# Optimization experiments

Measured on AMD Instinct MI355X. Metric: run time of the kernel, lower is better.

Reference implementation:

```python
import jax, jax.numpy as jnp
import numpy as np

B, T, D, H = 8, 4096, 1024, 64


def setup_inputs() -> dict:
    key = jax.random.key(0)
    ks = jax.random.split(key, 16)
    s = 0.02
    return {
        "x": jax.random.normal(ks[0], (B, T, D), jnp.float32),
        "norm_w": jnp.ones((D,), jnp.float32),
        "W1": jax.random.normal(ks[1], (D, D), jnp.float32) * s,
        "W2": jax.random.normal(ks[2], (D, D), jnp.float32) * s,
        "Wlast": jax.random.normal(ks[3], (D, D), jnp.float32) * s,
        "conv_w": jax.random.normal(ks[4], (D, 3), jnp.float32) * s,  # depthwise k=3, tap 0 = oldest
        "conv_b": jnp.zeros((D,), jnp.float32),
        "A": jnp.log(jnp.arange(1, H + 1, dtype=jnp.float32)),
        "Bw": jax.random.normal(ks[5], (H, D), jnp.float32) * s,
        "Bb": jnp.zeros((H,), jnp.float32),
        "Cw": jax.random.normal(ks[6], (D, H), jnp.float32) * s,
        "Cb": jnp.zeros((D,), jnp.float32),
        "Dw": jax.random.normal(ks[7], (D, D), jnp.float32) * s,
        "Db": jnp.zeros((D,), jnp.float32),
        "dw": jax.random.normal(ks[8], (H, D), jnp.float32) * s,
        "db": jnp.zeros((H,), jnp.float32),
    }


def reference(x, norm_w, W1, W2, Wlast, conv_w, conv_b, A, Bw, Bb, Cw, Cb, Dw, Db, dw, db):
    eps = jnp.finfo(x.dtype).eps  # torch RMSNorm default eps
    res = x
    xn = x * jax.lax.rsqrt(jnp.mean(x * x, axis=-1, keepdims=True) + eps) * norm_w
    x_b = xn @ W1.T
    z = xn @ W2.T
    # causal depthwise conv, kernel_size=3, left-pad 2
    xp = jnp.pad(x_b, ((0, 0), (2, 0), (0, 0)))
    xc = xp[:, :-2] * conv_w[:, 0] + xp[:, 1:-1] * conv_w[:, 1] + xp[:, 2:] * conv_w[:, 2] + conv_b
    xc = jax.nn.silu(xc)
    # log-space selective scan (cumprod(exp(A)) == exp(cumsum(A)))
    delta = jax.nn.softplus(xc @ dw.T + db)          # (B,T,H)
    A_log = -jax.nn.softplus(A)                      # (H,)
    A_bar_log = delta * A_log
    B_bar = delta * (xc @ Bw.T + Bb)
    A_cum = jnp.clip(jnp.cumsum(A_bar_log, axis=1), -20.0, 20.0)
    A_shift = jnp.concatenate([jnp.zeros_like(A_cum[:, :1]), A_cum[:, :-1]], axis=1)
    h = jnp.exp(A_cum) * jnp.cumsum(B_bar * jnp.exp(-A_shift), axis=1)
    y = h @ Cw.T + Cb + (xc @ Dw.T + Db)
    out = (y * jax.nn.silu(z)) @ Wlast.T + res
    return out
```

## Files before the change

kernel.cpp:

```cpp
#include <hip/hip_runtime.h>
#include <stdint.h>
#include <stddef.h>

#define TDIM 4096
#define DDIM 1024
#define HDIM 64
#define BDIM 8
#define MROWS (BDIM * TDIM)
#define KCAT (DDIM + HDIM)

typedef unsigned short ushort_t;
typedef __attribute__((ext_vector_type(8))) short short8;
typedef __attribute__((ext_vector_type(4))) float floatx4;

__device__ __forceinline__ unsigned short f2bf(float f) {
  unsigned u = __float_as_uint(f);
  u += 0x7fffu + ((u >> 16) & 1u);
  return (unsigned short)(u >> 16);
}
__device__ __forceinline__ float bf2f(unsigned short s) {
  return __uint_as_float(((unsigned)s) << 16);
}
__device__ __forceinline__ float softplusf(float x) {
  return x > 20.f ? x : log1pf(expf(x));
}

__global__ void k_cvt(const float* __restrict__ src, ushort_t* __restrict__ dst, int n) {
  int i = blockIdx.x * blockDim.x + threadIdx.x;
  if (i < n) dst[i] = f2bf(src[i]);
}

__global__ void k_bcat(const float* __restrict__ Dw, const float* __restrict__ Cw,
                       ushort_t* __restrict__ bcat) {
  int i = blockIdx.x * blockDim.x + threadIdx.x;
  if (i >= DDIM * KCAT) return;
  int row = i / KCAT, k = i - row * KCAT;
  float v = (k < DDIM) ? Dw[row * DDIM + k] : Cw[row * HDIM + (k - DDIM)];
  bcat[i] = f2bf(v);
}

__global__ void k_bias(const float* __restrict__ Cb, const float* __restrict__ Db,
                       float* __restrict__ biasCD) {
  int i = blockIdx.x * blockDim.x + threadIdx.x;
  if (i < DDIM) biasCD[i] = Cb[i] + Db[i];
}

__global__ __launch_bounds__(256) void k_rms(const float* __restrict__ x,
                                             const float* __restrict__ nw,
                                             ushort_t* __restrict__ xn) {
  const int row = blockIdx.x;
  const int tid = threadIdx.x;
  const size_t base = (size_t)row * DDIM + tid * 4;
  const float4 xv = *(const float4*)(x + base);
  float ss = xv.x * xv.x + xv.y * xv.y + xv.z * xv.z + xv.w * xv.w;
  for (int off = 32; off > 0; off >>= 1) ss += __shfl_down(ss, off, 64);
  __shared__ float sws[4];
  const int lane = tid & 63, w = tid >> 6;
  if (lane == 0) sws[w] = ss;
  __syncthreads();
  const float tot = sws[0] + sws[1] + sws[2] + sws[3];
  const float scale = rsqrtf(tot * (1.0f / DDIM) + 1.1920929e-7f);
  const float4 nwv = *(const float4*)(nw + tid * 4);
  ushort4 o;
  o.x = f2bf(xv.x * scale * nwv.x);
  o.y = f2bf(xv.y * scale * nwv.y);
  o.z = f2bf(xv.z * scale * nwv.z);
  o.w = f2bf(xv.w * scale * nwv.w);
  *(ushort4*)(xn + base) = o;
}

__global__ __launch_bounds__(256) void k_conv(const ushort_t* __restrict__ xz,
                                              const float* __restrict__ cw,
                                              const float* __restrict__ cb,
                                              ushort_t* __restrict__ acat) {
  const size_t idx = (size_t)blockIdx.x * 256 + threadIdx.x;
  const int d = (int)(idx & (DDIM - 1));
  const size_t m = idx >> 10;
  const int t = (int)(m & (TDIM - 1));
  const size_t s = m * 2048 + d;
  const float w0 = cw[d * 3 + 0], w1 = cw[d * 3 + 1], w2 = cw[d * 3 + 2];
  float v = bf2f(xz[s]) * w2;
  if (t >= 1) v += bf2f(xz[s - 2048]) * w1;
  if (t >= 2) v += bf2f(xz[s - 4096]) * w0;
  v += cb[d];
  const float sv = v / (1.f + __expf(-v));
  acat[m * KCAT + d] = f2bf(sv);
}

__global__ __launch_bounds__(256) void k_scan(const float* __restrict__ preG,
                                              const float* __restrict__ db,
                                              const float* __restrict__ Bb,
                                              const float* __restrict__ A,
                                              ushort_t* __restrict__ hT) {
  const int ch = blockIdx.x;
  const int b = ch >> 6, h = ch & 63;
  const int tid = threadIdx.x;
  const float dbh = db[h], Bbh = Bb[h];
  const float al = -softplusf(A[h]);
  const size_t base = ((size_t)b * TDIM + (size_t)tid * 16) * 128 + h;

  float a[16], bbv[16];
#pragma unroll
  for (int k = 0; k < 16; ++k) {
    const float p1 = preG[base + (size_t)k * 128];
    const float p2 = preG[base + (size_t)k * 128 + 64];
    const float delta = softplusf(p1 + dbh);
    a[k] = delta * al;
    bbv[k] = delta * (p2 + Bbh);
  }
  float run = 0.f;
#pragma unroll
  for (int k = 0; k < 16; ++k) { run += a[k]; a[k] = run; }

  __shared__ float sh[256];
  sh[tid] = run;
  __syncthreads();
  for (int s = 1; s < 256; s <<= 1) {
    float v = (tid >= s) ? sh[tid - s] : 0.f;
    __syncthreads();
    sh[tid] += v;
    __syncthreads();
  }
  const float off = (tid > 0) ? sh[tid - 1] : 0.f;
  __syncthreads();

  float term[16];
  float prev = off;
#pragma unroll
  for (int k = 0; k < 16; ++k) {
    const float Pk = off + a[k];
    const float Ashift = fminf(fmaxf(prev, -20.f), 20.f);
    term[k] = bbv[k] * expf(-Ashift);
    a[k] = fminf(fmaxf(Pk, -20.f), 20.f);
    prev = Pk;
  }

  float run2 = 0.f;
#pragma unroll
  for (int k = 0; k < 16; ++k) { run2 += term[k]; term[k] = run2; }
  sh[tid] = run2;
  __syncthreads();
  for (int s = 1; s < 256; s <<= 1) {
    float v = (tid >= s) ? sh[tid - s] : 0.f;
    __syncthreads();
    sh[tid] += v;
    __syncthreads();
  }
  const float off2 = (tid > 0) ? sh[tid - 1] : 0.f;

  ushort_t* dst = hT + (size_t)h * MROWS + (size_t)b * TDIM + (size_t)tid * 16;
#pragma unroll
  for (int k = 0; k < 16; ++k) {
    dst[k] = f2bf(expf(a[k]) * (off2 + term[k]));
  }
}

__global__ __launch_bounds__(256) void k_htrans(const ushort_t* __restrict__ hT,
                                                ushort_t* __restrict__ acat) {
  __shared__ ushort_t t[64 * 256];
  const int tid = threadIdx.x;
  const int m0 = blockIdx.x * 256;
#pragma unroll
  for (int p = 0; p < 8; ++p) {
    const int e = p * 2048 + tid * 8;
    const int h = e >> 8, mm = e & 255;
    *(short8*)(t + e) = *(const short8*)(hT + (size_t)h * MROWS + m0 + mm);
  }
  __syncthreads();
  ushort_t* dst = acat + (size_t)(m0 + tid) * KCAT + DDIM;
#pragma unroll
  for (int p = 0; p < 8; ++p) {
    short8 v;
#pragma unroll
    for (int e = 0; e < 8; ++e) v[e] = t[(p * 8 + e) * 256 + tid];
    *(short8*)(dst + p * 8) = v;
  }
}

__device__ __forceinline__ void stage128x64(const ushort_t* __restrict__ G, int row0,
                                            int ld, int kc, ushort_t* s, int wave, int lane) {
  const int rsub = lane >> 3;
  const int cpos = lane & 7;
  using gp_t = const unsigned int __attribute__((address_space(1)))*;
  using lp_t = unsigned int __attribute__((address_space(3)))*;
#pragma unroll
  for (int g = 0; g < 4; ++g) {
    const int rg = wave * 4 + g;
    const int r = rg * 8 + rsub;
    const int c = cpos ^ rsub;
    const ushort_t* src = G + (size_t)(row0 + r) * (size_t)ld + (size_t)(kc + c * 8);
    __builtin_amdgcn_global_load_lds((gp_t)(const void*)src, (lp_t)(void*)(s + rg * 512),
                                     16, 0, 0);
  }
}

__global__ __launch_bounds__(256, 3) void k_gemm(
    const ushort_t* __restrict__ A, int lda,
    const ushort_t* __restrict__ Bt, int ldb,
    int nB, int Kdim, int mode,
    float* __restrict__ outF, ushort_t* __restrict__ outB, int ldc,
    const float* __restrict__ bias,
    const ushort_t* __restrict__ zmat, int ldz,
    const float* __restrict__ resid) {
  __shared__ alignas(16) ushort_t smem[128 * 128];
  ushort_t* sA = smem;
  ushort_t* sB = smem + 128 * 64;
  const int tid = threadIdx.x;
  const int wave = tid >> 6, lane = tid & 63;

  const int per = gridDim.x >> 3;
  const int xcd = blockIdx.x & 7, slot = blockIdx.x >> 3;
  const int tile = xcd * per + slot;
  const int m0 = (tile / nB) * 128, n0 = (tile % nB) * 128;

  const int half_m = (wave & 1) * 64, half_n = (wave >> 1) * 64;
  const int quad = lane >> 4, l16 = lane & 15;

  floatx4 acc[4][4];
#pragma unroll
  for (int i = 0; i < 4; ++i)
#pragma unroll
    for (int j = 0; j < 4; ++j) acc[i][j] = floatx4{0.f, 0.f, 0.f, 0.f};

  for (int kc = 0; kc < Kdim; kc += 64) {
    stage128x64(A, m0, lda, kc, sA, wave, lane);
    stage128x64(Bt, n0, ldb, kc, sB, wave, lane);
    __syncthreads();
#pragma unroll
    for (int s = 0; s < 2; ++s) {
      short8 af[4], bfr[4];
#pragma unroll
      for (int i = 0; i < 4; ++i) {
        const int r = half_m + i * 16 + l16;
        const int cp = (s * 4 + quad) ^ (r & 7);
        af[i] = *(const short8*)(sA + r * 64 + cp * 8);
      }
#pragma unroll
      for (int j = 0; j < 4; ++j) {
        const int r = half_n + j * 16 + l16;
        const int cp = (s * 4 + quad) ^ (r & 7);
        bfr[j] = *(const short8*)(sB + r * 64 + cp * 8);
      }
#pragma unroll
      for (int i = 0; i < 4; ++i)
#pragma unroll
        for (int j = 0; j < 4; ++j)
          acc[i][j] = __builtin_amdgcn_mfma_f32_16x16x32_bf16(af[i], bfr[j], acc[i][j], 0, 0, 0);
    }
    __syncthreads();
  }

#pragma unroll
  for (int i = 0; i < 4; ++i)
#pragma unroll
    for (int j = 0; j < 4; ++j)
#pragma unroll
      for (int rg = 0; rg < 4; ++rg) {
        const int r = half_m + i * 16 + quad * 4 + rg;
        const int c = half_n + j * 16 + l16;
        smem[r * 128 + c] = f2bf(acc[i][j][rg]);
      }
  __syncthreads();

#pragma unroll
  for (int p = 0; p < 8; ++p) {
    const int r = p * 16 + (tid >> 4);
    const int c = (tid & 15) * 8;
    short8 v8 = *(const short8*)(smem + r * 128 + c);
    const size_t m = (size_t)(m0 + r);
    const int n = n0 + c;
    if (mode == 0) {
      *(short8*)(outB + m * (size_t)ldc + n) = v8;
    } else if (mode == 1) {
      float* o = outF + m * (size_t)ldc + n;
#pragma unroll
      for (int e = 0; e < 8; ++e) o[e] = bf2f((ushort_t)v8[e]);
    } else if (mode == 2) {
      const short8 z8 = *(const short8*)(zmat + m * (size_t)ldz + n);
      short8 o;
#pragma unroll
      for (int e = 0; e < 8; ++e) {
        const float v = bf2f((ushort_t)v8[e]) + bias[n + e];
        const float zf = bf2f((ushort_t)z8[e]);
        o[e] = (short)f2bf(v * (zf / (1.f + __expf(-zf))));
      }
      *(short8*)(outB + m * (size_t)ldc + n) = o;
    } else {
      const float* rs = resid + m * (size_t)ldc + n;
      float* o = outF + m * (size_t)ldc + n;
#pragma unroll
      for (int e = 0; e < 8; ++e) o[e] = bf2f((ushort_t)v8[e]) + rs[e];
    }
  }
}

extern "C" void kernel_launch(void* const* d_in, const int* in_sizes, int n_in,
                              void* d_out, int out_size, void* d_ws, size_t ws_size,
                              hipStream_t stream) {
  const float* x      = (const float*)d_in[0];
  const float* norm_w = (const float*)d_in[1];
  const float* W1     = (const float*)d_in[2];
  const float* W2     = (const float*)d_in[3];
  const float* Wlast  = (const float*)d_in[4];
  const float* conv_w = (const float*)d_in[5];
  const float* conv_b = (const float*)d_in[6];
  const float* Aarr   = (const float*)d_in[7];
  const float* Bw     = (const float*)d_in[8];
  const float* Bb     = (const float*)d_in[9];
  const float* Cw     = (const float*)d_in[10];
  const float* Cb     = (const float*)d_in[11];
  const float* Dw     = (const float*)d_in[12];
  const float* Db     = (const float*)d_in[13];
  const float* dwm    = (const float*)d_in[14];
  const float* dbv    = (const float*)d_in[15];

  char* ws = (char*)d_ws;
  ushort_t* xz   = (ushort_t*)(ws + 0);
  ushort_t* acat = (ushort_t*)(ws + 134217728);
  float*   preG  = (float*)(ws + 205520896);
  ushort_t* hT   = (ushort_t*)(ws + 222298112);
  ushort_t* xnu  = (ushort_t*)(ws + 226492416);
  ushort_t* wcat = (ushort_t*)(ws + 293601280);
  ushort_t* wlb  = (ushort_t*)(ws + 297795584);
  ushort_t* dwbw = (ushort_t*)(ws + 299892736);
  ushort_t* bcat = (ushort_t*)(ws + 300154880);
  float*  biasCD = (float*)(ws + 302383104);
  float*   outF  = (float*)d_out;

  k_cvt<<<4096, 256, 0, stream>>>(W1, wcat, DDIM * DDIM);
  k_cvt<<<4096, 256, 0, stream>>>(W2, wcat + DDIM * DDIM, DDIM * DDIM);
  k_cvt<<<4096, 256, 0, stream>>>(Wlast, wlb, DDIM * DDIM);
  k_cvt<<<256, 256, 0, stream>>>(dwm, dwbw, HDIM * DDIM);
  k_cvt<<<256, 256, 0, stream>>>(Bw, dwbw + HDIM * DDIM, HDIM * DDIM);
  k_bcat<<<(DDIM * KCAT + 255) / 256, 256, 0, stream>>>(Dw, Cw, bcat);
  k_bias<<<4, 256, 0, stream>>>(Cb, Db, biasCD);

  k_rms<<<MROWS, 256, 0, stream>>>(x, norm_w, xnu);

  k_gemm<<<256 * 16, 256, 0, stream>>>(xnu, DDIM, wcat, DDIM, 16, DDIM, 0,
                                       nullptr, xz, 2048, nullptr, nullptr, 0, nullptr);

  k_conv<<<(MROWS * DDIM) / 256, 256, 0, stream>>>(xz, conv_w, conv_b, acat);

  k_gemm<<<256 * 1, 256, 0, stream>>>(acat, KCAT, dwbw, DDIM, 1, DDIM, 1,
                                      preG, nullptr, 128, nullptr, nullptr, 0, nullptr);

  k_scan<<<BDIM * HDIM, 256, 0, stream>>>(preG, dbv, Bb, Aarr, hT);

  k_htrans<<<MROWS / 256, 256, 0, stream>>>(hT, acat);

  k_gemm<<<256 * 8, 256, 0, stream>>>(acat, KCAT, bcat, KCAT, 8, KCAT, 2,
                                      nullptr, xnu, DDIM, biasCD, xz + DDIM, 2048, nullptr);

  k_gemm<<<256 * 8, 256, 0, stream>>>(xnu, DDIM, wlb, DDIM, 8, DDIM, 3,
                                      outF, nullptr, DDIM, nullptr, nullptr, 0, x);

  (void)in_sizes; (void)n_in; (void)out_size; (void)ws_size;
}
```

Baseline: 761.8 us.

## Fuse weight prep, vectorize conv, transpose delta/B GEMM output, raise occupancy

Merges the seven weight-conversion and bias launches into one prep kernel. Vectorizes the depthwise conv to process eight channels per thread with 16-byte loads and stores. Swaps the operands of the small delta/B projection GEMM so its output is laid out channel-major (H x M), which lets the scan read contiguous float4s instead of strided scalars. It also raises the GEMM launch-bounds occupancy hint from 3 to 4 blocks per SIMD, which may increase register pressure or spills in the large GEMMs.

```diff
diff --git a/kernel.cpp b/kernel.cpp
--- a/kernel.cpp
+++ b/kernel.cpp
@@ -8,6 +8,8 @@
 #define BDIM 8
 #define MROWS (BDIM * TDIM)
 #define KCAT (DDIM + HDIM)
+#define DD (DDIM * DDIM)
+#define HD (HDIM * DDIM)
 
 typedef unsigned short ushort_t;
 typedef __attribute__((ext_vector_type(8))) short short8;
@@ -25,23 +27,32 @@
   return x > 20.f ? x : log1pf(expf(x));
 }
 
-__global__ void k_cvt(const float* __restrict__ src, ushort_t* __restrict__ dst, int n) {
-  int i = blockIdx.x * blockDim.x + threadIdx.x;
-  if (i < n) dst[i] = f2bf(src[i]);
-}
-
-__global__ void k_bcat(const float* __restrict__ Dw, const float* __restrict__ Cw,
-                       ushort_t* __restrict__ bcat) {
-  int i = blockIdx.x * blockDim.x + threadIdx.x;
-  if (i >= DDIM * KCAT) return;
-  int row = i / KCAT, k = i - row * KCAT;
-  float v = (k < DDIM) ? Dw[row * DDIM + k] : Cw[row * HDIM + (k - DDIM)];
-  bcat[i] = f2bf(v);
-}
-
-__global__ void k_bias(const float* __restrict__ Cb, const float* __restrict__ Db,
+__global__ void k_prep(const float* __restrict__ W1, const float* __restrict__ W2,
+                       const float* __restrict__ Wlast, const float* __restrict__ dwm,
+                       const float* __restrict__ Bw, const float* __restrict__ Dw,
+                       const float* __restrict__ Cw, const float* __restrict__ Cb,
+                       const float* __restrict__ Db,
+                       ushort_t* __restrict__ wcat, ushort_t* __restrict__ wlb,
+                       ushort_t* __restrict__ dwbw, ushort_t* __restrict__ bcat,
                        float* __restrict__ biasCD) {
-  int i = blockIdx.x * blockDim.x + threadIdx.x;
+  int i = blockIdx.x * 256 + threadIdx.x;
+  if (i < DD) { wcat[i] = f2bf(W1[i]); return; }
+  i -= DD;
+  if (i < DD) { wcat[DD + i] = f2bf(W2[i]); return; }
+  i -= DD;
+  if (i < DD) { wlb[i] = f2bf(Wlast[i]); return; }
+  i -= DD;
+  if (i < HD) { dwbw[i] = f2bf(dwm[i]); return; }
+  i -= HD;
+  if (i < HD) { dwbw[HD + i] = f2bf(Bw[i]); return; }
+  i -= HD;
+  if (i < DDIM * KCAT) {
+    const int row = i / KCAT, k = i - row * KCAT;
+    const float v = (k < DDIM) ? Dw[row * DDIM + k] : Cw[row * HDIM + (k - DDIM)];
+    bcat[i] = f2bf(v);
+    return;
+  }
+  i -= DDIM * KCAT;
   if (i < DDIM) biasCD[i] = Cb[i] + Db[i];
 }
 
@@ -73,18 +84,26 @@
                                               const float* __restrict__ cw,
                                               const float* __restrict__ cb,
                                               ushort_t* __restrict__ acat) {
-  const size_t idx = (size_t)blockIdx.x * 256 + threadIdx.x;
-  const int d = (int)(idx & (DDIM - 1));
-  const size_t m = idx >> 10;
+  const size_t eidx = ((size_t)blockIdx.x * 256 + threadIdx.x) * 8;
+  const int d = (int)(eidx & (DDIM - 1));
+  const size_t m = eidx >> 10;
   const int t = (int)(m & (TDIM - 1));
   const size_t s = m * 2048 + d;
-  const float w0 = cw[d * 3 + 0], w1 = cw[d * 3 + 1], w2 = cw[d * 3 + 2];
-  float v = bf2f(xz[s]) * w2;
-  if (t >= 1) v += bf2f(xz[s - 2048]) * w1;
-  if (t >= 2) v += bf2f(xz[s - 4096]) * w0;
-  v += cb[d];
-  const float sv = v / (1.f + __expf(-v));
-  acat[m * KCAT + d] = f2bf(sv);
+  const short8 r2 = *(const short8*)(xz + s);
+  short8 r1 = {0,0,0,0,0,0,0,0}, r0 = {0,0,0,0,0,0,0,0};
+  if (t >= 1) r1 = *(const short8*)(xz + s - 2048);
+  if (t >= 2) r0 = *(const short8*)(xz + s - 4096);
+  short8 o;
+#pragma unroll
+  for (int e = 0; e < 8; ++e) {
+    const int de = d + e;
+    float v = bf2f((ushort_t)r2[e]) * cw[de * 3 + 2]
+            + bf2f((ushort_t)r1[e]) * cw[de * 3 + 1]
+            + bf2f((ushort_t)r0[e]) * cw[de * 3 + 0]
+            + cb[de];
+    o[e] = (short)f2bf(v / (1.f + __expf(-v)));
+  }
+  *(short8*)(acat + m * KCAT + d) = o;
 }
 
 __global__ __launch_bounds__(256) void k_scan(const float* __restrict__ preG,
@@ -97,16 +116,22 @@
   const int tid = threadIdx.x;
   const float dbh = db[h], Bbh = Bb[h];
   const float al = -softplusf(A[h]);
-  const size_t base = ((size_t)b * TDIM + (size_t)tid * 16) * 128 + h;
+  const size_t base1 = (size_t)h * MROWS + (size_t)b * TDIM + (size_t)tid * 16;
+  const size_t base2 = base1 + (size_t)64 * MROWS;
 
   float a[16], bbv[16];
 #pragma unroll
-  for (int k = 0; k < 16; ++k) {
-    const float p1 = preG[base + (size_t)k * 128];
-    const float p2 = preG[base + (size_t)k * 128 + 64];
-    const float delta = softplusf(p1 + dbh);
-    a[k] = delta * al;
-    bbv[k] = delta * (p2 + Bbh);
+  for (int k4 = 0; k4 < 4; ++k4) {
+    const float4 p1 = *(const float4*)(preG + base1 + k4 * 4);
+    const float4 p2 = *(const float4*)(preG + base2 + k4 * 4);
+    const float pp1[4] = {p1.x, p1.y, p1.z, p1.w};
+    const float pp2[4] = {p2.x, p2.y, p2.z, p2.w};
+#pragma unroll
+    for (int e = 0; e < 4; ++e) {
+      const float delta = softplusf(pp1[e] + dbh);
+      a[k4 * 4 + e] = delta * al;
+      bbv[k4 * 4 + e] = delta * (pp2[e] + Bbh);
+    }
   }
   float run = 0.f;
 #pragma unroll
@@ -194,7 +219,7 @@
   }
 }
 
-__global__ __launch_bounds__(256, 3) void k_gemm(
+__global__ __launch_bounds__(256, 4) void k_gemm(
     const ushort_t* __restrict__ A, int lda,
     const ushort_t* __restrict__ Bt, int ldb,
     int nB, int Kdim, int mode,
@@ -327,23 +352,21 @@
   float*  biasCD = (float*)(ws + 302383104);
   float*   outF  = (float*)d_out;
 
-  k_cvt<<<4096, 256, 0, stream>>>(W1, wcat, DDIM * DDIM);
-  k_cvt<<<4096, 256, 0, stream>>>(W2, wcat + DDIM * DDIM, DDIM * DDIM);
-  k_cvt<<<4096, 256, 0, stream>>>(Wlast, wlb, DDIM * DDIM);
-  k_cvt<<<256, 256, 0, stream>>>(dwm, dwbw, HDIM * DDIM);
-  k_cvt<<<256, 256, 0, stream>>>(Bw, dwbw + HDIM * DDIM, HDIM * DDIM);
-  k_bcat<<<(DDIM * KCAT + 255) / 256, 256, 0, stream>>>(Dw, Cw, bcat);
-  k_bias<<<4, 256, 0, stream>>>(Cb, Db, biasCD);
+  {
+    const int total = 3 * DD + 2 * HD + DDIM * KCAT + DDIM;
+    k_prep<<<(total + 255) / 256, 256, 0, stream>>>(W1, W2, Wlast, dwm, Bw, Dw, Cw, Cb, Db,
+                                                    wcat, wlb, dwbw, bcat, biasCD);
+  }
 
   k_rms<<<MROWS, 256, 0, stream>>>(x, norm_w, xnu);
 
   k_gemm<<<256 * 16, 256, 0, stream>>>(xnu, DDIM, wcat, DDIM, 16, DDIM, 0,
                                        nullptr, xz, 2048, nullptr, nullptr, 0, nullptr);
 
-  k_conv<<<(MROWS * DDIM) / 256, 256, 0, stream>>>(xz, conv_w, conv_b, acat);
-
-  k_gemm<<<256 * 1, 256, 0, stream>>>(acat, KCAT, dwbw, DDIM, 1, DDIM, 1,
-                                      preG, nullptr, 128, nullptr, nullptr, 0, nullptr);
+  k_conv<<<(MROWS * DDIM) / (256 * 8), 256, 0, stream>>>(xz, conv_w, conv_b, acat);
+
+  k_gemm<<<256, 256, 0, stream>>>(dwbw, DDIM, acat, KCAT, 256, DDIM, 1,
+                                  preG, nullptr, MROWS, nullptr, nullptr, 0, nullptr);
 
   k_scan<<<BDIM * HDIM, 256, 0, stream>>>(preG, dbv, Bb, Aarr, hT);
 
```

Result: faster. 682.1 us (-10.5%).
